# Kernel optimization log

Measured on AMD Instinct MI355X. Metric: run time of the kernel, lower is better.

The kernel has to match this reference:

```python
import jax, jax.numpy as jnp
import numpy as np


def setup_inputs() -> dict:
    key = jax.random.key(0)
    ks = jax.random.split(key, 7)
    B, C, H, W = 2, 8, 80, 80  # planes=8 -> planes//8 = 1 reduced channel
    Cr = C // 8
    x = jax.random.normal(ks[0], (B, C, H, W), jnp.float32)
    w1 = jax.random.normal(ks[1], (Cr, C), jnp.float32) * 0.1
    b1 = jax.random.normal(ks[2], (Cr,), jnp.float32) * 0.1
    w2 = jax.random.normal(ks[3], (Cr, C), jnp.float32) * 0.1
    b2 = jax.random.normal(ks[4], (Cr,), jnp.float32) * 0.1
    w3 = jax.random.normal(ks[5], (Cr, C), jnp.float32) * 0.1
    b3 = jax.random.normal(ks[6], (Cr,), jnp.float32) * 0.1
    return {"x": x, "w1": w1, "b1": b1, "w2": w2, "b2": b2, "w3": w3, "b3": b3}


def reference(x, w1, b1, w2, b2, w3, b3):
    B, C, H, W = x.shape
    N = H * W

    def conv1x1(w, b):
        # 1x1 conv == per-pixel channel projection; flatten spatial to N
        return (jnp.einsum('bchw,oc->bohw', x, w) + b[None, :, None, None]).reshape(B, -1, N)

    f1 = conv1x1(w1, b1)  # (B, Cr, N) query-like
    f2 = conv1x1(w2, b2)  # (B, Cr, N) key-like
    f3 = conv1x1(w3, b3)  # (B, Cr, N) value-like
    # f2^T @ f1 -> (B, N, N), softmax over last dim (no scaling, per original)
    attn = jax.nn.softmax(jnp.einsum('bcn,bcm->bnm', f2, f1), axis=-1)
    # f3 @ attn^T -> (B, Cr, N); Cr == 1 so reshape to (B,1,H,W)
    gate = jax.nn.sigmoid(jnp.einsum('bcn,bmn->bcm', f3, attn))
    return x * gate.reshape(B, 1, H, W)
```

## Files before the change

### kernel.cpp

```cpp
#include <hip/hip_runtime.h>
#include <hip/hip_bf16.h>

#define BB 2
#define CC 8
#define NN 6400

__global__ void proj_kernel(const float* __restrict__ x,
                            const float* __restrict__ w1, const float* __restrict__ b1,
                            const float* __restrict__ w2, const float* __restrict__ b2,
                            const float* __restrict__ w3, const float* __restrict__ b3,
                            float* __restrict__ f1, float* __restrict__ f2, float* __restrict__ f3) {
    int i = blockIdx.x * blockDim.x + threadIdx.x;
    if (i >= BB * NN) return;
    int b = i / NN;
    int n = i - b * NN;
    const float* xp = x + (size_t)b * CC * NN + n;
    float a1 = b1[0];
    float a2 = b2[0];
    float a3 = b3[0];
#pragma unroll
    for (int c = 0; c < CC; ++c) {
        float xv = xp[(size_t)c * NN];
        a1 = fmaf(xv, w1[c], a1);
        a2 = fmaf(xv, w2[c], a2);
        a3 = fmaf(xv, w3[c], a3);
    }
    f1[i] = a1;
    f2[i] = a2;
    f3[i] = a3;
}

__global__ void attn_kernel(const float* __restrict__ f1, const float* __restrict__ f2,
                            const float* __restrict__ f3,
                            float* __restrict__ pnum, float* __restrict__ pden,
                            int chunkLen) {
    extern __shared__ float sm[];
    float* s1 = sm;
    float* s3 = sm + chunkLen;
    const int b  = blockIdx.z;
    const int ch = blockIdx.y;
    const int m  = blockIdx.x * blockDim.x + threadIdx.x;
    const int base = b * NN + ch * chunkLen;
    for (int j = threadIdx.x; j < chunkLen; j += blockDim.x) {
        s1[j] = f1[base + j];
        s3[j] = f3[base + j];
    }
    __syncthreads();
    if (m >= NN) return;
    const float s = f2[b * NN + m] * 1.4426950408889634f;
    float num = 0.f, den = 0.f;
#pragma unroll 4
    for (int j = 0; j < chunkLen; ++j) {
        float e = __builtin_amdgcn_exp2f(s * s1[j]);
        num = fmaf(s3[j], e, num);
        den += e;
    }
    const size_t o = (size_t)(ch * BB + b) * NN + m;
    pnum[o] = num;
    pden[o] = den;
}

__global__ void finish_kernel(const float* __restrict__ x,
                              const float* __restrict__ pnum, const float* __restrict__ pden,
                              float* __restrict__ out, int nchunk) {
    int i = blockIdx.x * blockDim.x + threadIdx.x;
    if (i >= BB * NN) return;
    int b = i / NN;
    int m = i - b * NN;
    float num = 0.f, den = 0.f;
    for (int ch = 0; ch < nchunk; ++ch) {
        size_t o = (size_t)(ch * BB + b) * NN + m;
        num += pnum[o];
        den += pden[o];
    }
    float g = num / den;
    float sig = 1.0f / (1.0f + __builtin_amdgcn_exp2f(-g * 1.4426950408889634f));
    const float* xp = x + (size_t)b * CC * NN + m;
    float* op = out + (size_t)b * CC * NN + m;
#pragma unroll
    for (int c = 0; c < CC; ++c) {
        op[(size_t)c * NN] = xp[(size_t)c * NN] * sig;
    }
}

extern "C" void kernel_launch(void* const* d_in, const int* in_sizes, int n_in,
                              void* d_out, int out_size, void* d_ws, size_t ws_size,
                              hipStream_t stream) {
    const float* x  = (const float*)d_in[0];
    const float* w1 = (const float*)d_in[1];
    const float* b1 = (const float*)d_in[2];
    const float* w2 = (const float*)d_in[3];
    const float* b2 = (const float*)d_in[4];
    const float* w3 = (const float*)d_in[5];
    const float* b3 = (const float*)d_in[6];
    float* out = (float*)d_out;

    float* ws = (float*)d_ws;
    const size_t BN = (size_t)BB * NN;

    int nchunk = 8;
    while (nchunk > 1 && (size_t)(3 + 2 * nchunk) * BN * sizeof(float) > ws_size) nchunk >>= 1;

    float* f1   = ws;
    float* f2   = ws + BN;
    float* f3   = ws + 2 * BN;
    float* pnum = ws + 3 * BN;
    float* pden = pnum + (size_t)nchunk * BN;

    const int threads = 256;
    const int blocksBN = (int)((BN + threads - 1) / threads);

    proj_kernel<<<blocksBN, threads, 0, stream>>>(x, w1, b1, w2, b2, w3, b3, f1, f2, f3);

    const int chunkLen = NN / nchunk;
    dim3 g2(NN / threads, nchunk, BB);
    attn_kernel<<<g2, threads, 2 * chunkLen * sizeof(float), stream>>>(f1, f2, f3, pnum, pden, chunkLen);

    finish_kernel<<<blocksBN, threads, 0, stream>>>(x, pnum, pden, out, nchunk);
}
```

Baseline: 91.98 us.

## Fuse projection into attention kernel with register-tiled queries and more chunks

Removes the separate projection kernel: each attention block computes its own key/value chunk (pre-scaled by log2e) into shared memory and its query projections directly from x. Each thread now handles four query positions, so every shared-memory load is reused four times. The key dimension is split into 64 chunks for more parallelism, and the finish kernel uses float4 loads. In exchange, query projection is recomputed once per chunk, the partial-sum buffers grow and there is more reduction traffic, and the code assumes the workspace is large enough without checking.

```diff
diff --git a/kernel.cpp b/kernel.cpp
--- a/kernel.cpp
+++ b/kernel.cpp
@@ -4,82 +4,115 @@
 #define BB 2
 #define CC 8
 #define NN 6400
+#define NCH 64
+#define CHLEN 100
+#define THR 320
+#define MPT 4
+#define MT (THR*MPT)
+#define LOG2E 1.4426950408889634f
 
-__global__ void proj_kernel(const float* __restrict__ x,
-                            const float* __restrict__ w1, const float* __restrict__ b1,
-                            const float* __restrict__ w2, const float* __restrict__ b2,
-                            const float* __restrict__ w3, const float* __restrict__ b3,
-                            float* __restrict__ f1, float* __restrict__ f2, float* __restrict__ f3) {
-    int i = blockIdx.x * blockDim.x + threadIdx.x;
-    if (i >= BB * NN) return;
-    int b = i / NN;
-    int n = i - b * NN;
-    const float* xp = x + (size_t)b * CC * NN + n;
-    float a1 = b1[0];
-    float a2 = b2[0];
-    float a3 = b3[0];
+__global__ __launch_bounds__(THR) void attn_fused(
+    const float* __restrict__ x,
+    const float* __restrict__ w1, const float* __restrict__ b1,
+    const float* __restrict__ w2, const float* __restrict__ b2,
+    const float* __restrict__ w3, const float* __restrict__ b3,
+    float* __restrict__ pnum, float* __restrict__ pden) {
+    __shared__ float4 s1v[CHLEN / 4];
+    __shared__ float4 s3v[CHLEN / 4];
+    const int b   = blockIdx.z;
+    const int ch  = blockIdx.y;
+    const int mt  = blockIdx.x;
+    const int tid = threadIdx.x;
+    const float* xb = x + (size_t)b * CC * NN;
+
+    if (tid < CHLEN) {
+        const int n = ch * CHLEN + tid;
+        float a1 = b1[0], a3 = b3[0];
+#pragma unroll
+        for (int c = 0; c < CC; ++c) {
+            float xv = xb[c * NN + n];
+            a1 = fmaf(xv, w1[c], a1);
+            a3 = fmaf(xv, w3[c], a3);
+        }
+        ((float*)s1v)[tid] = a1 * LOG2E;
+        ((float*)s3v)[tid] = a3;
+    }
+
+    const int m0 = mt * MT + tid * MPT;
+    float sc[MPT];
+    {
+        float bb2 = b2[0];
+#pragma unroll
+        for (int i = 0; i < MPT; ++i) sc[i] = bb2;
+#pragma unroll
+        for (int c = 0; c < CC; ++c) {
+            const float wc = w2[c];
+            const float4 xq = *(const float4*)(xb + (size_t)c * NN + m0);
+            sc[0] = fmaf(xq.x, wc, sc[0]);
+            sc[1] = fmaf(xq.y, wc, sc[1]);
+            sc[2] = fmaf(xq.z, wc, sc[2]);
+            sc[3] = fmaf(xq.w, wc, sc[3]);
+        }
+    }
+    __syncthreads();
+
+    float num[MPT] = {0.f, 0.f, 0.f, 0.f};
+    float den[MPT] = {0.f, 0.f, 0.f, 0.f};
+#pragma unroll 5
+    for (int jj = 0; jj < CHLEN / 4; ++jj) {
+        const float4 v1 = s1v[jj];
+        const float4 v3 = s3v[jj];
+        const float e1a[4] = {v1.x, v1.y, v1.z, v1.w};
+        const float e3a[4] = {v3.x, v3.y, v3.z, v3.w};
+#pragma unroll
+        for (int k = 0; k < 4; ++k) {
+            const float f1k = e1a[k];
+            const float f3k = e3a[k];
+#pragma unroll
+            for (int i = 0; i < MPT; ++i) {
+                const float e = __builtin_amdgcn_exp2f(sc[i] * f1k);
+                num[i] = fmaf(f3k, e, num[i]);
+                den[i] += e;
+            }
+        }
+    }
+
+    const size_t o = (size_t)(ch * BB + b) * NN + m0;
+    *(float4*)(pnum + o) = make_float4(num[0], num[1], num[2], num[3]);
+    *(float4*)(pden + o) = make_float4(den[0], den[1], den[2], den[3]);
+}
+
+__global__ __launch_bounds__(64) void finish_kernel(
+    const float* __restrict__ x,
+    const float* __restrict__ pnum, const float* __restrict__ pden,
+    float* __restrict__ out) {
+    const int t  = blockIdx.x * blockDim.x + threadIdx.x;
+    const int bm = t * 4;
+    const int b  = bm / NN;
+    const int m0 = bm - b * NN;
+    float num[4] = {0.f, 0.f, 0.f, 0.f};
+    float den[4] = {0.f, 0.f, 0.f, 0.f};
+#pragma unroll 8
+    for (int ch = 0; ch < NCH; ++ch) {
+        const size_t o = (size_t)(ch * BB + b) * NN + m0;
+        const float4 a = *(const float4*)(pnum + o);
+        const float4 d = *(const float4*)(pden + o);
+        num[0] += a.x; num[1] += a.y; num[2] += a.z; num[3] += a.w;
+        den[0] += d.x; den[1] += d.y; den[2] += d.z; den[3] += d.w;
+    }
+    float sig[4];
+#pragma unroll
+    for (int i = 0; i < 4; ++i) {
+        const float g = num[i] / den[i];
+        sig[i] = 1.0f / (1.0f + __builtin_amdgcn_exp2f(-g * LOG2E));
+    }
+    const float* xb = x + (size_t)b * CC * NN + m0;
+    float* ob = out + (size_t)b * CC * NN + m0;
 #pragma unroll
     for (int c = 0; c < CC; ++c) {
-        float xv = xp[(size_t)c * NN];
-        a1 = fmaf(xv, w1[c], a1);
-        a2 = fmaf(xv, w2[c], a2);
-        a3 = fmaf(xv, w3[c], a3);
-    }
-    f1[i] = a1;
-    f2[i] = a2;
-    f3[i] = a3;
-}
-
-__global__ void attn_kernel(const float* __restrict__ f1, const float* __restrict__ f2,
-                            const float* __restrict__ f3,
-                            float* __restrict__ pnum, float* __restrict__ pden,
-                            int chunkLen) {
-    extern __shared__ float sm[];
-    float* s1 = sm;
-    float* s3 = sm + chunkLen;
-    const int b  = blockIdx.z;
-    const int ch = blockIdx.y;
-    const int m  = blockIdx.x * blockDim.x + threadIdx.x;
-    const int base = b * NN + ch * chunkLen;
-    for (int j = threadIdx.x; j < chunkLen; j += blockDim.x) {
-        s1[j] = f1[base + j];
-        s3[j] = f3[base + j];
-    }
-    __syncthreads();
-    if (m >= NN) return;
-    const float s = f2[b * NN + m] * 1.4426950408889634f;
-    float num = 0.f, den = 0.f;
-#pragma unroll 4
-    for (int j = 0; j < chunkLen; ++j) {
-        float e = __builtin_amdgcn_exp2f(s * s1[j]);
-        num = fmaf(s3[j], e, num);
-        den += e;
-    }
-    const size_t o = (size_t)(ch * BB + b) * NN + m;
-    pnum[o] = num;
-    pden[o] = den;
-}
-
-__global__ void finish_kernel(const float* __restrict__ x,
-                              const float* __restrict__ pnum, const float* __restrict__ pden,
-                              float* __restrict__ out, int nchunk) {
-    int i = blockIdx.x * blockDim.x + threadIdx.x;
-    if (i >= BB * NN) return;
-    int b = i / NN;
-    int m = i - b * NN;
-    float num = 0.f, den = 0.f;
-    for (int ch = 0; ch < nchunk; ++ch) {
-        size_t o = (size_t)(ch * BB + b) * NN + m;
-        num += pnum[o];
-        den += pden[o];
-    }
-    float g = num / den;
-    float sig = 1.0f / (1.0f + __builtin_amdgcn_exp2f(-g * 1.4426950408889634f));
-    const float* xp = x + (size_t)b * CC * NN + m;
-    float* op = out + (size_t)b * CC * NN + m;
-#pragma unroll
-    for (int c = 0; c < CC; ++c) {
-        op[(size_t)c * NN] = xp[(size_t)c * NN] * sig;
+        const float4 xq = *(const float4*)(xb + (size_t)c * NN);
+        *(float4*)(ob + (size_t)c * NN) =
+            make_float4(xq.x * sig[0], xq.y * sig[1], xq.z * sig[2], xq.w * sig[3]);
     }
 }
 
@@ -97,24 +130,11 @@
 
     float* ws = (float*)d_ws;
     const size_t BN = (size_t)BB * NN;
+    float* pnum = ws;
+    float* pden = ws + (size_t)NCH * BN;
 
-    int nchunk = 8;
-    while (nchunk > 1 && (size_t)(3 + 2 * nchunk) * BN * sizeof(float) > ws_size) nchunk >>= 1;
+    dim3 g2(NN / MT, NCH, BB);
+    attn_fused<<<g2, THR, 0, stream>>>(x, w1, b1, w2, b2, w3, b3, pnum, pden);
 
-    float* f1   = ws;
-    float* f2   = ws + BN;
-    float* f3   = ws + 2 * BN;
-    float* pnum = ws + 3 * BN;
-    float* pden = pnum + (size_t)nchunk * BN;
-
-    const int threads = 256;
-    const int blocksBN = (int)((BN + threads - 1) / threads);
-
-    proj_kernel<<<blocksBN, threads, 0, stream>>>(x, w1, b1, w2, b2, w3, b3, f1, f2, f3);
-
-    const int chunkLen = NN / nchunk;
-    dim3 g2(NN / threads, nchunk, BB);
-    attn_kernel<<<g2, threads, 2 * chunkLen * sizeof(float), stream>>>(f1, f2, f3, pnum, pden, chunkLen);
-
-    finish_kernel<<<blocksBN, threads, 0, stream>>>(x, pnum, pden, out, nchunk);
+    finish_kernel<<<(int)(BN / 4 / 64), 64, 0, stream>>>(x, pnum, pden, out);
 }
```

Result: no change. 90.27 us (-1.9%).
